# Kernel tuning notes

Hardware: AMD Instinct MI355X
Metric: run time of the kernel (lower is better)

The kernel has to match this reference:

```python
import jax, jax.numpy as jnp
import numpy as np

N_NODES = 100000
N_EDGES = 1000000


def setup_inputs() -> dict:
    key = jax.random.key(0)
    ks = jax.random.split(key, 8)
    x = jax.random.normal(ks[0], (N_NODES, 58), dtype=jnp.float32)
    edge_index = jax.random.randint(ks[1], (2, N_EDGES), 0, N_NODES, dtype=jnp.int64)
    # Glorot-ish scaled weights
    W1 = jax.random.normal(ks[2], (58, 300), dtype=jnp.float32) * (1.0 / np.sqrt(58))
    b1 = jnp.zeros((300,), dtype=jnp.float32)
    W2 = jax.random.normal(ks[3], (300, 100), dtype=jnp.float32) * (1.0 / np.sqrt(300))
    b2 = jnp.zeros((100,), dtype=jnp.float32)
    W3 = jax.random.normal(ks[4], (100, 1), dtype=jnp.float32) * (1.0 / np.sqrt(100))
    b3 = jnp.zeros((1,), dtype=jnp.float32)
    return {"x": x, "edge_index": edge_index, "W1": W1, "b1": b1,
            "W2": W2, "b2": b2, "W3": W3, "b3": b3}


def _gcn_norm(edge_index, num_nodes):
    # add self-loops, then symmetric normalization D^-1/2 A D^-1/2 (PyG gcn_norm)
    ar = jnp.arange(num_nodes, dtype=edge_index.dtype)
    ei = jnp.concatenate([edge_index, jnp.stack([ar, ar])], axis=1)
    row, col = ei[0], ei[1]
    deg = jax.ops.segment_sum(jnp.ones(row.shape[0], dtype=jnp.float32), col,
                              num_segments=num_nodes)
    dis = jnp.where(deg > 0, jax.lax.rsqrt(jnp.maximum(deg, 1.0)), 0.0)
    norm = dis[row] * dis[col]  # [E]
    return row, col, norm


def _gcn_conv(x, W, b, row, col, norm, num_nodes):
    h = x @ W                                  # [N, F_out]
    msg = h[row] * norm[:, None]               # gather + per-edge scale
    agg = jax.ops.segment_sum(msg, col, num_segments=num_nodes)  # scatter-add
    return agg + b


def reference(x, edge_index, W1, b1, W2, b2, W3, b3):
    n = x.shape[0]
    row, col, norm = _gcn_norm(edge_index, n)
    # eval mode: F.dropout(training=False) is identity
    h = jax.nn.relu(_gcn_conv(x, W1, b1, row, col, norm, n))
    h = jax.nn.relu(_gcn_conv(h, W2, b2, row, col, norm, n))
    out = _gcn_conv(h, W3, b3, row, col, norm, n)
    return out
```

## Files before the change

### kernel.cpp

```cpp
#include <hip/hip_runtime.h>
#include <hip/hip_bf16.h>

typedef __hip_bfloat16 bf16;
typedef __attribute__((ext_vector_type(8))) short s8v;
typedef __attribute__((ext_vector_type(4))) float f4v;

#define CAP 40

template <int MODE>
__device__ __forceinline__ float ld_m(const void* p, long long i, int dynbf) {
    if (MODE == 0) return ((const float*)p)[i];
    if (MODE == 1) return __bfloat162float(((const bf16*)p)[i]);
    return dynbf ? __bfloat162float(((const bf16*)p)[i]) : ((const float*)p)[i];
}
template <int MODE>
__device__ __forceinline__ void st_m(void* p, long long i, float v, int dynbf) {
    if (MODE == 0) { ((float*)p)[i] = v; return; }
    if (MODE == 1) { ((bf16*)p)[i] = __float2bfloat16(v); return; }
    if (dynbf) ((bf16*)p)[i] = __float2bfloat16(v);
    else       ((float*)p)[i] = v;
}

__device__ __forceinline__ float relu_keepnan(float v) { return (v <= 0.f) ? 0.f : v; }
__device__ __forceinline__ int clampi(int v, int lo, int hi) {
    return v < lo ? lo : (v > hi ? hi : v);
}
__device__ __forceinline__ short f2bf_bits(float v) {
    bf16 h = __float2bfloat16(v);
    return *(short*)&h;
}
__device__ __forceinline__ float bflo(unsigned w) { return __uint_as_float(w << 16); }
__device__ __forceinline__ float bfhi(unsigned w) { return __uint_as_float(w & 0xffff0000u); }
__device__ __forceinline__ unsigned pack2(float a, float b) {
    return ((unsigned)(unsigned short)f2bf_bits(a)) | (((unsigned)(unsigned short)f2bf_bits(b)) << 16);
}

__global__ void k_init(int* __restrict__ cnt, int n,
                       const int* __restrict__ ei, const unsigned* __restrict__ xw,
                       int* __restrict__ flags) {
    int i = blockIdx.x * blockDim.x + threadIdx.x;
    int stride = gridDim.x * blockDim.x;
    for (int j = i; j < n; j += stride) cnt[j] = 0;
    if (blockIdx.x == 0 && threadIdx.x < 64) {
        int lane = threadIdx.x;
        int ov = (lane < 16) ? ei[2 * lane + 1] : 0;
        unsigned long long be = __ballot(ov != 0);
        int inb = 0;
        #pragma unroll
        for (int q = 0; q < 2; ++q) {
            unsigned w = xw[lane + 64 * q];
            int e = (w >> 7) & 0xFF;
            inb += (e >= 110 && e <= 131) ? 1 : 0;
        }
        #pragma unroll
        for (int o = 32; o; o >>= 1) inb += __shfl_down(inb, o, 64);
        if (lane == 0) {
            flags[0] = (be == 0ULL) ? 1 : 0;
            flags[1] = (inb >= 64) ? 1 : 0;
        }
    }
}

__global__ void k_fill_prep(const int* __restrict__ ei, int* __restrict__ cnt,
                            int* __restrict__ csr_row, int E, int n, int psz, int CH,
                            int cblocks,
                            const void* __restrict__ x, const void* __restrict__ W1,
                            const void* __restrict__ W2, ushort* __restrict__ xq,
                            short* __restrict__ W1t, short* __restrict__ W2t,
                            const int* __restrict__ flags) {
    if ((int)blockIdx.x < cblocks) {
        int c = blockIdx.x >> 3;
        int p = blockIdx.x & 7;
        bool i64 = flags[0] != 0;
        const int plo = p * psz;
        const unsigned pun = (unsigned)psz;
        int lo = c * CH;
        int hi = lo + CH; if (hi > E) hi = E;
        const bool alOK = i64 ? ((E & 1) == 0) : ((E & 3) == 0);
        const int* cb32 = ei + E;
        const int* cb64 = ei + 2LL * E;
        for (int e = lo + threadIdx.x * 4; e < hi; e += 1024) {
            int cols[4];
            int m = hi - e; if (m > 4) m = 4;
            if (m == 4 && alOK) {
                if (i64) {
                    uint4 cv0 = *(const uint4*)(cb64 + 2LL * e);
                    uint4 cv1 = *(const uint4*)(cb64 + 2LL * e + 4);
                    cols[0] = (int)cv0.x; cols[1] = (int)cv0.z;
                    cols[2] = (int)cv1.x; cols[3] = (int)cv1.z;
                } else {
                    uint4 cv = *(const uint4*)(cb32 + e);
                    cols[0] = (int)cv.x; cols[1] = (int)cv.y;
                    cols[2] = (int)cv.z; cols[3] = (int)cv.w;
                }
            } else {
                #pragma unroll
                for (int j = 0; j < 4; ++j)
                    cols[j] = (j < m) ? (i64 ? cb64[2LL * (e + j)] : cb32[e + j])
                                      : -1;
            }
            #pragma unroll
            for (int j = 0; j < 4; ++j) {
                if (j >= m) continue;
                int col = clampi(cols[j], 0, n - 1);
                if ((unsigned)(col - plo) >= pun) continue;
                int r = ei[i64 ? 2LL * (e + j) : (long long)(e + j)];
                r = clampi(r, 0, n - 1);
                int pos = atomicAdd(&cnt[col], 1);
                if (pos >= 0 && pos < CAP) csr_row[(long long)col * CAP + pos] = r;
            }
        }
        return;
    }
    int fbf = flags[1];
    long long idx = (long long)(blockIdx.x - cblocks) * blockDim.x + threadIdx.x;
    long long nx8 = (long long)n * 8;
    if (idx < nx8) {
        int i = (int)(idx >> 3), f8 = (int)(idx & 7);
        int f = f8 * 8;
        uint4 outw;
        if (f8 < 7) {
            if (fbf) {
                const uint* up = (const uint*)((const ushort*)x + (long long)i * 58 + f);
                outw.x = up[0]; outw.y = up[1]; outw.z = up[2]; outw.w = up[3];
            } else {
                const float* xp = (const float*)x + (long long)i * 58 + f;
                float2 v0 = *(const float2*)(xp + 0);
                float2 v1 = *(const float2*)(xp + 2);
                float2 v2 = *(const float2*)(xp + 4);
                float2 v3 = *(const float2*)(xp + 6);
                outw.x = pack2(v0.x, v0.y);
                outw.y = pack2(v1.x, v1.y);
                outw.z = pack2(v2.x, v2.y);
                outw.w = pack2(v3.x, v3.y);
            }
        } else {
            if (fbf) {
                const uint* up = (const uint*)((const ushort*)x + (long long)i * 58 + 56);
                outw.x = up[0];
            } else {
                const float* xp = (const float*)x + (long long)i * 58 + 56;
                outw.x = pack2(xp[0], xp[1]);
            }
            outw.y = 0u; outw.z = 0u; outw.w = 0u;
        }
        *(uint4*)&xq[(long long)i * 64 + f] = outw;
        return;
    }
    long long j = idx - nx8;
    if (j < 320 * 64) {
        int nn = (int)(j >> 6), k = (int)(j & 63);
        float v = (nn < 300 && k < 58) ? ld_m<2>(W1, (long long)k * 300 + nn, fbf) : 0.f;
        W1t[j] = f2bf_bits(v);
        return;
    }
    long long j2 = j - 320 * 64;
    if (j2 < 128 * 320) {
        int nn = (int)(j2 / 320), k = (int)(j2 - (long long)nn * 320);
        float v = (nn < 100 && k < 300) ? ld_m<2>(W2, (long long)k * 100 + nn, fbf) : 0.f;
        W2t[j2] = f2bf_bits(v);
    }
}

__global__ void k_dis(const int* __restrict__ cnt, float* __restrict__ dis, int n) {
    int i = blockIdx.x * blockDim.x + threadIdx.x;
    if (i < n) dis[i] = rsqrtf(fmaxf((float)(cnt[i] + 1), 1.0f));
}

template <int OPN>
__global__ void k_aggo_pre(const uint4* __restrict__ src, uint4* __restrict__ dst,
                           const int* __restrict__ cnt, const int* __restrict__ csr_row,
                           const float* __restrict__ dis, int n) {
    long long idx = (long long)blockIdx.x * blockDim.x + threadIdx.x;
    if (idx >= (long long)n * OPN) return;
    int i = (int)(idx / OPN);
    int o = (int)(idx - (long long)i * OPN);
    float di = dis[i];
    uint4 sw = src[(long long)i * OPN + o];
    float a[8];
    a[0] = bflo(sw.x) * di; a[1] = bfhi(sw.x) * di;
    a[2] = bflo(sw.y) * di; a[3] = bfhi(sw.y) * di;
    a[4] = bflo(sw.z) * di; a[5] = bfhi(sw.z) * di;
    a[6] = bflo(sw.w) * di; a[7] = bfhi(sw.w) * di;
    int deg = cnt[i]; deg = clampi(deg, 0, CAP);
    int e0 = i * CAP;
    int e1 = e0 + deg;
    int e = e0;
    for (; e + 8 <= e1; e += 8) {
        int r[8];
        uint4 w[8];
        float d[8];
        #pragma unroll
        for (int j = 0; j < 8; ++j) r[j] = clampi(csr_row[e + j], 0, n - 1);
        #pragma unroll
        for (int j = 0; j < 8; ++j) w[j] = src[(long long)r[j] * OPN + o];
        #pragma unroll
        for (int j = 0; j < 8; ++j) d[j] = dis[r[j]];
        #pragma unroll
        for (int j = 0; j < 8; ++j) {
            a[0] = fmaf(bflo(w[j].x), d[j], a[0]);
            a[1] = fmaf(bfhi(w[j].x), d[j], a[1]);
            a[2] = fmaf(bflo(w[j].y), d[j], a[2]);
            a[3] = fmaf(bfhi(w[j].y), d[j], a[3]);
            a[4] = fmaf(bflo(w[j].z), d[j], a[4]);
            a[5] = fmaf(bfhi(w[j].z), d[j], a[5]);
            a[6] = fmaf(bflo(w[j].w), d[j], a[6]);
            a[7] = fmaf(bfhi(w[j].w), d[j], a[7]);
        }
    }
    for (; e + 4 <= e1; e += 4) {
        int r[4];
        uint4 w[4];
        float d[4];
        #pragma unroll
        for (int j = 0; j < 4; ++j) r[j] = clampi(csr_row[e + j], 0, n - 1);
        #pragma unroll
        for (int j = 0; j < 4; ++j) w[j] = src[(long long)r[j] * OPN + o];
        #pragma unroll
        for (int j = 0; j < 4; ++j) d[j] = dis[r[j]];
        #pragma unroll
        for (int j = 0; j < 4; ++j) {
            a[0] = fmaf(bflo(w[j].x), d[j], a[0]);
            a[1] = fmaf(bfhi(w[j].x), d[j], a[1]);
            a[2] = fmaf(bflo(w[j].y), d[j], a[2]);
            a[3] = fmaf(bfhi(w[j].y), d[j], a[3]);
            a[4] = fmaf(bflo(w[j].z), d[j], a[4]);
            a[5] = fmaf(bfhi(w[j].z), d[j], a[5]);
            a[6] = fmaf(bflo(w[j].w), d[j], a[6]);
            a[7] = fmaf(bfhi(w[j].w), d[j], a[7]);
        }
    }
    for (; e < e1; ++e) {
        int r = clampi(csr_row[e], 0, n - 1);
        uint4 w = src[(long long)r * OPN + o];
        float d = dis[r];
        a[0] = fmaf(bflo(w.x), d, a[0]);
        a[1] = fmaf(bfhi(w.x), d, a[1]);
        a[2] = fmaf(bflo(w.y), d, a[2]);
        a[3] = fmaf(bfhi(w.y), d, a[3]);
        a[4] = fmaf(bflo(w.z), d, a[4]);
        a[5] = fmaf(bfhi(w.z), d, a[5]);
        a[6] = fmaf(bflo(w.w), d, a[6]);
        a[7] = fmaf(bfhi(w.w), d, a[7]);
    }
    uint4 outw;
    outw.x = pack2(di * a[0], di * a[1]);
    outw.y = pack2(di * a[2], di * a[3]);
    outw.z = pack2(di * a[4], di * a[5]);
    outw.w = pack2(di * a[6], di * a[7]);
    dst[(long long)i * OPN + o] = outw;
}

template <int QPN>
__global__ void k_aggq_fused(const uint2* __restrict__ src, float* __restrict__ t3,
                             const int* __restrict__ cnt, const int* __restrict__ csr_row,
                             const float* __restrict__ dis, const void* __restrict__ b2,
                             const void* __restrict__ W3, int n,
                             const int* __restrict__ flags) {
    __shared__ float sdata[256];
    int tid = threadIdx.x;
    int ln = tid / QPN;
    int q = tid - ln * QPN;
    int node = blockIdx.x * 10 + ln;
    bool active = (tid < 10 * QPN) && (node < n);
    int fbf = flags[1];
    float partial = 0.f;
    float di = 0.f;
    if (active) {
        di = dis[node];
        uint2 sw = src[(long long)node * QPN + q];
        float a0 = bflo(sw.x), a1 = bfhi(sw.x), a2 = bflo(sw.y), a3 = bfhi(sw.y);
        int deg = cnt[node]; deg = clampi(deg, 0, CAP);
        int e0 = node * CAP;
        int e1 = e0 + deg;
        int e = e0;
        for (; e + 8 <= e1; e += 8) {
            int r[8];
            uint2 w[8];
            #pragma unroll
            for (int j = 0; j < 8; ++j) r[j] = clampi(csr_row[e + j], 0, n - 1);
            #pragma unroll
            for (int j = 0; j < 8; ++j) w[j] = src[(long long)r[j] * QPN + q];
            #pragma unroll
            for (int j = 0; j < 8; ++j) {
                a0 += bflo(w[j].x); a1 += bfhi(w[j].x);
                a2 += bflo(w[j].y); a3 += bfhi(w[j].y);
            }
        }
        for (; e + 4 <= e1; e += 4) {
            int r0 = clampi(csr_row[e],     0, n - 1);
            int r1 = clampi(csr_row[e + 1], 0, n - 1);
            int r2 = clampi(csr_row[e + 2], 0, n - 1);
            int r3 = clampi(csr_row[e + 3], 0, n - 1);
            uint2 w0 = src[(long long)r0 * QPN + q];
            uint2 w1 = src[(long long)r1 * QPN + q];
            uint2 w2 = src[(long long)r2 * QPN + q];
            uint2 w3 = src[(long long)r3 * QPN + q];
            a0 += bflo(w0.x) + bflo(w1.x) + bflo(w2.x) + bflo(w3.x);
            a1 += bfhi(w0.x) + bfhi(w1.x) + bfhi(w2.x) + bfhi(w3.x);
            a2 += bflo(w0.y) + bflo(w1.y) + bflo(w2.y) + bflo(w3.y);
            a3 += bfhi(w0.y) + bfhi(w1.y) + bfhi(w2.y) + bfhi(w3.y);
        }
        for (; e < e1; ++e) {
            int r = clampi(csr_row[e], 0, n - 1);
            uint2 w = src[(long long)r * QPN + q];
            a0 += bflo(w.x); a1 += bfhi(w.x); a2 += bflo(w.y); a3 += bfhi(w.y);
        }
        float o0 = relu_keepnan(di * a0 + ld_m<2>(b2, 4 * q + 0, fbf));
        float o1 = relu_keepnan(di * a1 + ld_m<2>(b2, 4 * q + 1, fbf));
        float o2 = relu_keepnan(di * a2 + ld_m<2>(b2, 4 * q + 2, fbf));
        float o3 = relu_keepnan(di * a3 + ld_m<2>(b2, 4 * q + 3, fbf));
        partial = o0 * ld_m<2>(W3, 4 * q + 0, fbf) + o1 * ld_m<2>(W3, 4 * q + 1, fbf)
                + o2 * ld_m<2>(W3, 4 * q + 2, fbf) + o3 * ld_m<2>(W3, 4 * q + 3, fbf);
    }
    sdata[tid] = partial;
    __syncthreads();
    if (active && q == 0) {
        float s = 0.f;
        #pragma unroll
        for (int j = 0; j < QPN; ++j) s += sdata[tid + j];
        t3[node] = di * s;
    }
}

__global__ void k_agg1(const float* __restrict__ src, void* __restrict__ dst,
                       const int* __restrict__ cnt, const int* __restrict__ csr_row,
                       const float* __restrict__ dis, const void* __restrict__ bias,
                       int n, const int* __restrict__ flags) {
    int i = blockIdx.x * blockDim.x + threadIdx.x;
    if (i >= n) return;
    int fbf = flags[1];
    float di = dis[i];
    float acc = src[i];
    int deg = cnt[i]; deg = clampi(deg, 0, CAP);
    int e0 = i * CAP;
    int e1 = e0 + deg;
    int e = e0;
    for (; e + 4 <= e1; e += 4) {
        int r0 = clampi(csr_row[e],     0, n - 1);
        int r1 = clampi(csr_row[e + 1], 0, n - 1);
        int r2 = clampi(csr_row[e + 2], 0, n - 1);
        int r3 = clampi(csr_row[e + 3], 0, n - 1);
        acc += src[r0] + src[r1] + src[r2] + src[r3];
    }
    for (; e < e1; ++e) {
        int r = clampi(csr_row[e], 0, n - 1);
        acc += src[r];
    }
    float out = di * acc + ld_m<2>(bias, 0, fbf);
    st_m<2>(dst, i, out, fbf);
}

template <int NT, bool SCALE_ROW, bool HAS_BIAS, bool RELU>
__global__ __launch_bounds__(256) void k_gemm_mfma(
    const ushort* __restrict__ A, const ushort* __restrict__ Bt,
    const void* __restrict__ bias, const float* __restrict__ dis,
    bf16* __restrict__ C, int M, int KP, int chunks, int ldc, int NBreal,
    const int* __restrict__ flags) {
    constexpr int BN = NT * 16;
    __shared__ __align__(16) ushort A_s[128][40];
    __shared__ __align__(16) ushort B_s[BN][40];
    const int t = threadIdx.x;
    const int lane = t & 63;
    const int w = t >> 6;
    const int bm = blockIdx.y * 128;
    const int bn = blockIdx.x * BN;
    const int fbf = flags[1];
    const int mrow = lane & 15;
    const int quad = lane >> 4;

    f4v acc[2][NT];
    #pragma unroll
    for (int a = 0; a < 2; a++)
        #pragma unroll
        for (int b = 0; b < NT; b++)
            #pragma unroll
            for (int r = 0; r < 4; r++) acc[a][b][r] = 0.f;

    for (int c = 0; c < chunks; ++c) {
        const int k0 = c * 32;
        #pragma unroll
        for (int r = 0; r < 2; ++r) {
            int u = t + r * 256;
            int row = u >> 2, kq = (u & 3) * 8;
            int grow = bm + row;
            uint4 v = make_uint4(0u, 0u, 0u, 0u);
            if (grow < M) v = *(const uint4*)(A + (size_t)grow * KP + k0 + kq);
            *(uint4*)&A_s[row][kq] = v;
        }
        for (int u = t; u < BN * 4; u += 256) {
            int row = u >> 2, kq = (u & 3) * 8;
            uint4 v = *(const uint4*)(Bt + (size_t)(bn + row) * KP + k0 + kq);
            *(uint4*)&B_s[row][kq] = v;
        }
        __syncthreads();
        s8v a0 = *(const s8v*)&A_s[w * 32 + mrow][quad * 8];
        s8v a1 = *(const s8v*)&A_s[w * 32 + 16 + mrow][quad * 8];
        #pragma unroll
        for (int nt = 0; nt < NT; ++nt) {
            s8v b = *(const s8v*)&B_s[nt * 16 + mrow][quad * 8];
            acc[0][nt] = __builtin_amdgcn_mfma_f32_16x16x32_bf16(a0, b, acc[0][nt], 0, 0, 0);
            acc[1][nt] = __builtin_amdgcn_mfma_f32_16x16x32_bf16(a1, b, acc[1][nt], 0, 0, 0);
        }
        __syncthreads();
    }
    float sc[2][4];
    #pragma unroll
    for (int mi = 0; mi < 2; ++mi)
        #pragma unroll
        for (int r = 0; r < 4; ++r) {
            int gm = bm + w * 32 + mi * 16 + quad * 4 + r;
            sc[mi][r] = (SCALE_ROW && gm < M) ? dis[gm] : 1.f;
        }
    #pragma unroll
    for (int nt = 0; nt < NT; ++nt) {
        int gn = bn + nt * 16 + mrow;
        if (gn >= ldc) continue;
        float bv = 0.f;
        if (HAS_BIAS) bv = (gn < NBreal) ? ld_m<2>(bias, gn, fbf) : 0.f;
        #pragma unroll
        for (int mi = 0; mi < 2; ++mi)
            #pragma unroll
            for (int r = 0; r < 4; ++r) {
                int gm = bm + w * 32 + mi * 16 + quad * 4 + r;
                if (gm >= M) continue;
                float v = acc[mi][nt][r] * sc[mi][r];
                if (HAS_BIAS) v += bv;
                if (RELU) v = relu_keepnan(v);
                C[(size_t)gm * ldc + gn] = __float2bfloat16(v);
            }
    }
}

extern "C" void kernel_launch(void* const* d_in, const int* in_sizes, int n_in,
                              void* d_out, int out_size, void* d_ws, size_t ws_size,
                              hipStream_t stream) {
    const void* x  = d_in[0];
    const int*  ei = (const int*)d_in[1];
    const void* W1 = d_in[2];
    const void* b1 = d_in[3];
    const void* W2 = d_in[4];
    const void* b2 = d_in[5];
    const void* W3 = d_in[6];
    const void* b3 = d_in[7];

    const int F0 = 58;
    const int N = in_sizes[0] / F0;
    const int E = in_sizes[1] / 2;
    const int gy = (N + 127) / 128;
    const int CH = 4096;
    const int NC = (E + CH - 1) / CH;
    const int psz = (N + 7) / 8;

    size_t off = 0;
    auto alloc = [&](size_t bytes) -> void* {
        void* p = (char*)d_ws + off;
        off = (off + bytes + 255) & ~(size_t)255;
        return p;
    };
    int*   flags   = (int*)alloc(256);
    int*   cnt     = (int*)alloc((size_t)N * 4);
    float* dis     = (float*)alloc((size_t)N * 4);
    int*   csr_row = (int*)alloc((size_t)N * CAP * 4);
    short* W1t     = (short*)alloc((size_t)320 * 64 * 2);
    short* W2t     = (short*)alloc((size_t)128 * 320 * 2);
    float* t3      = (float*)alloc((size_t)N * 4);
    void*  regA    = alloc((size_t)N * 128 * 2);
    ushort* z_bf = (ushort*)regA;
    bf16*   t2   = (bf16*)regA;
    void*  regB    = alloc((size_t)N * 320 * 2);
    ushort* xq = (ushort*)regB;
    bf16*   h1 = (bf16*)regB;

    k_init<<<1024, 256, 0, stream>>>(cnt, N, ei, (const unsigned*)x, flags);
    {
        int cblocks = NC * 8;
        long long ptot = (long long)N * 8 + 320 * 64 + 128 * 320;
        int pblocks = (int)((ptot + 255) / 256);
        k_fill_prep<<<cblocks + pblocks, 256, 0, stream>>>(
            ei, cnt, csr_row, E, N, psz, CH, cblocks, x, W1, W2, xq, W1t, W2t, flags);
    }
    k_dis<<<(N + 255) / 256, 256, 0, stream>>>(cnt, dis, N);

    k_aggo_pre<8><<<((long long)N * 8 + 255) / 256, 256, 0, stream>>>(
        (const uint4*)xq, (uint4*)z_bf, cnt, csr_row, dis, N);
    k_gemm_mfma<10, false, true, true><<<dim3(2, gy), 256, 0, stream>>>(
        z_bf, (const ushort*)W1t, b1, dis, h1, N, 64, 2, 320, 300, flags);

    k_gemm_mfma<8, true, false, false><<<dim3(1, gy), 256, 0, stream>>>(
        (const ushort*)h1, (const ushort*)W2t, nullptr, dis, t2, N, 320, 10, 100, 0, flags);
    k_aggq_fused<25><<<(N + 9) / 10, 256, 0, stream>>>(
        (const uint2*)t2, t3, cnt, csr_row, dis, b2, W3, N, flags);

    k_agg1<<<(N + 255) / 256, 256, 0, stream>>>(
        t3, d_out, cnt, csr_row, dis, b3, N, flags);
}
```

Baseline: 309.9 us.

## Pad layer-2 output to 128 columns and aggregate with 16-byte loads and shuffles

```diff
diff --git a/kernel.cpp b/kernel.cpp
--- a/kernel.cpp
+++ b/kernel.cpp
@@ -251,76 +251,81 @@
     dst[(long long)i * OPN + o] = outw;
 }
 
-template <int QPN>
-__global__ void k_aggq_fused(const uint2* __restrict__ src, float* __restrict__ t3,
+__global__ void k_aggq_fused(const uint4* __restrict__ src, float* __restrict__ t3,
                              const int* __restrict__ cnt, const int* __restrict__ csr_row,
                              const float* __restrict__ dis, const void* __restrict__ b2,
                              const void* __restrict__ W3, int n,
                              const int* __restrict__ flags) {
-    __shared__ float sdata[256];
     int tid = threadIdx.x;
-    int ln = tid / QPN;
-    int q = tid - ln * QPN;
-    int node = blockIdx.x * 10 + ln;
-    bool active = (tid < 10 * QPN) && (node < n);
+    int ln = tid >> 4;
+    int q  = tid & 15;
+    int node = blockIdx.x * 16 + ln;
+    if (node >= n) return;
     int fbf = flags[1];
+    float di = dis[node];
+    uint4 sw = src[(long long)node * 16 + q];
+    float a[8];
+    a[0] = bflo(sw.x); a[1] = bfhi(sw.x);
+    a[2] = bflo(sw.y); a[3] = bfhi(sw.y);
+    a[4] = bflo(sw.z); a[5] = bfhi(sw.z);
+    a[6] = bflo(sw.w); a[7] = bfhi(sw.w);
+    int deg = cnt[node]; deg = clampi(deg, 0, CAP);
+    int e0 = node * CAP;
+    int e1 = e0 + deg;
+    int e = e0;
+    for (; e + 8 <= e1; e += 8) {
+        int r[8];
+        uint4 w[8];
+        #pragma unroll
+        for (int j = 0; j < 8; ++j) r[j] = clampi(csr_row[e + j], 0, n - 1);
+        #pragma unroll
+        for (int j = 0; j < 8; ++j) w[j] = src[(long long)r[j] * 16 + q];
+        #pragma unroll
+        for (int j = 0; j < 8; ++j) {
+            a[0] += bflo(w[j].x); a[1] += bfhi(w[j].x);
+            a[2] += bflo(w[j].y); a[3] += bfhi(w[j].y);
+            a[4] += bflo(w[j].z); a[5] += bfhi(w[j].z);
+            a[6] += bflo(w[j].w); a[7] += bfhi(w[j].w);
+        }
+    }
+    for (; e + 4 <= e1; e += 4) {
+        int r[4];
+        uint4 w[4];
+        #pragma unroll
+        for (int j = 0; j < 4; ++j) r[j] = clampi(csr_row[e + j], 0, n - 1);
+        #pragma unroll
+        for (int j = 0; j < 4; ++j) w[j] = src[(long long)r[j] * 16 + q];
+        #pragma unroll
+        for (int j = 0; j < 4; ++j) {
+            a[0] += bflo(w[j].x); a[1] += bfhi(w[j].x);
+            a[2] += bflo(w[j].y); a[3] += bfhi(w[j].y);
+            a[4] += bflo(w[j].z); a[5] += bfhi(w[j].z);
+            a[6] += bflo(w[j].w); a[7] += bfhi(w[j].w);
+        }
+    }
+    for (; e < e1; ++e) {
+        int r = clampi(csr_row[e], 0, n - 1);
+        uint4 w = src[(long long)r * 16 + q];
+        a[0] += bflo(w.x); a[1] += bfhi(w.x);
+        a[2] += bflo(w.y); a[3] += bfhi(w.y);
+        a[4] += bflo(w.z); a[5] += bfhi(w.z);
+        a[6] += bflo(w.w); a[7] += bfhi(w.w);
+    }
+    int base = q * 8;
     float partial = 0.f;
-    float di = 0.f;
-    if (active) {
-        di = dis[node];
-        uint2 sw = src[(long long)node * QPN + q];
-        float a0 = bflo(sw.x), a1 = bfhi(sw.x), a2 = bflo(sw.y), a3 = bfhi(sw.y);
-        int deg = cnt[node]; deg = clampi(deg, 0, CAP);
-        int e0 = node * CAP;
-        int e1 = e0 + deg;
-        int e = e0;
-        for (; e + 8 <= e1; e += 8) {
-            int r[8];
-            uint2 w[8];
-            #pragma unroll
-            for (int j = 0; j < 8; ++j) r[j] = clampi(csr_row[e + j], 0, n - 1);
-            #pragma unroll
-            for (int j = 0; j < 8; ++j) w[j] = src[(long long)r[j] * QPN + q];
-            #pragma unroll
-            for (int j = 0; j < 8; ++j) {
-                a0 += bflo(w[j].x); a1 += bfhi(w[j].x);
-                a2 += bflo(w[j].y); a3 += bfhi(w[j].y);
-            }
-        }
-        for (; e + 4 <= e1; e += 4) {
-            int r0 = clampi(csr_row[e],     0, n - 1);
-            int r1 = clampi(csr_row[e + 1], 0, n - 1);
-            int r2 = clampi(csr_row[e + 2], 0, n - 1);
-            int r3 = clampi(csr_row[e + 3], 0, n - 1);
-            uint2 w0 = src[(long long)r0 * QPN + q];
-            uint2 w1 = src[(long long)r1 * QPN + q];
-            uint2 w2 = src[(long long)r2 * QPN + q];
-            uint2 w3 = src[(long long)r3 * QPN + q];
-            a0 += bflo(w0.x) + bflo(w1.x) + bflo(w2.x) + bflo(w3.x);
-            a1 += bfhi(w0.x) + bfhi(w1.x) + bfhi(w2.x) + bfhi(w3.x);
-            a2 += bflo(w0.y) + bflo(w1.y) + bflo(w2.y) + bflo(w3.y);
-            a3 += bfhi(w0.y) + bfhi(w1.y) + bfhi(w2.y) + bfhi(w3.y);
-        }
-        for (; e < e1; ++e) {
-            int r = clampi(csr_row[e], 0, n - 1);
-            uint2 w = src[(long long)r * QPN + q];
-            a0 += bflo(w.x); a1 += bfhi(w.x); a2 += bflo(w.y); a3 += bfhi(w.y);
-        }
-        float o0 = relu_keepnan(di * a0 + ld_m<2>(b2, 4 * q + 0, fbf));
-        float o1 = relu_keepnan(di * a1 + ld_m<2>(b2, 4 * q + 1, fbf));
-        float o2 = relu_keepnan(di * a2 + ld_m<2>(b2, 4 * q + 2, fbf));
-        float o3 = relu_keepnan(di * a3 + ld_m<2>(b2, 4 * q + 3, fbf));
-        partial = o0 * ld_m<2>(W3, 4 * q + 0, fbf) + o1 * ld_m<2>(W3, 4 * q + 1, fbf)
-                + o2 * ld_m<2>(W3, 4 * q + 2, fbf) + o3 * ld_m<2>(W3, 4 * q + 3, fbf);
-    }
-    sdata[tid] = partial;
-    __syncthreads();
-    if (active && q == 0) {
-        float s = 0.f;
-        #pragma unroll
-        for (int j = 0; j < QPN; ++j) s += sdata[tid + j];
-        t3[node] = di * s;
-    }
+    #pragma unroll
+    for (int k = 0; k < 8; ++k) {
+        int el = base + k;
+        if (el < 100) {
+            float o = relu_keepnan(di * a[k] + ld_m<2>(b2, el, fbf));
+            partial += o * ld_m<2>(W3, el, fbf);
+        }
+    }
+    partial += __shfl_xor(partial, 8, 64);
+    partial += __shfl_xor(partial, 4, 64);
+    partial += __shfl_xor(partial, 2, 64);
+    partial += __shfl_xor(partial, 1, 64);
+    if (q == 0) t3[node] = di * partial;
 }
 
 __global__ void k_agg1(const float* __restrict__ src, void* __restrict__ dst,
@@ -488,9 +493,9 @@
         z_bf, (const ushort*)W1t, b1, dis, h1, N, 64, 2, 320, 300, flags);
 
     k_gemm_mfma<8, true, false, false><<<dim3(1, gy), 256, 0, stream>>>(
-        (const ushort*)h1, (const ushort*)W2t, nullptr, dis, t2, N, 320, 10, 100, 0, flags);
-    k_aggq_fused<25><<<(N + 9) / 10, 256, 0, stream>>>(
-        (const uint2*)t2, t3, cnt, csr_row, dis, b2, W3, N, flags);
+        (const ushort*)h1, (const ushort*)W2t, nullptr, dis, t2, N, 320, 10, 128, 0, flags);
+    k_aggq_fused<<<(N + 15) / 16, 256, 0, stream>>>(
+        (const uint4*)t2, t3, cnt, csr_row, dis, b2, W3, N, flags);
 
     k_agg1<<<(N + 255) / 256, 256, 0, stream>>>(
         t3, d_out, cnt, csr_row, dis, b3, N, flags);
```

After: 325.9 us. 1.05x slower.
